# Kernel optimization log

Measured on AMD Instinct MI355X. Metric: run time of the kernel, lower is better.

The kernel has to match this reference:

```python
import jax, jax.numpy as jnp
import numpy as np

N = 100_000      # nodes
E = 1_600_000    # edges (avg degree 16)
D_IN = 128
D_OUT = 128
K = 64           # low-rank attention rank


def setup_inputs() -> dict:
    key = jax.random.key(0)
    ks = jax.random.split(key, 6)
    s = lambda d: 1.0 / np.sqrt(d)
    return {
        "x": jax.random.normal(ks[0], (N, D_IN), dtype=jnp.float32),
        "edge_index": jax.random.randint(ks[1], (2, E), 0, N, dtype=jnp.int32),
        "W_gcn": jax.random.normal(ks[2], (D_IN, D_OUT), dtype=jnp.float32) * s(D_IN),
        "b_gcn": jnp.zeros((D_OUT,), jnp.float32),
        "W_att": jax.random.normal(ks[3], (D_IN, 4 * K), dtype=jnp.float32) * s(D_IN),
        "b_att": jnp.zeros((4 * K,), jnp.float32),
        "W_red": jax.random.normal(ks[4], (D_OUT + 2 * K, D_OUT), dtype=jnp.float32) * s(D_OUT + 2 * K),
        "b_red": jnp.zeros((D_OUT,), jnp.float32),
    }


def _forward(x, W_gcn, b_gcn, W_att, b_att, W_red, b_red, edge_index):
    n = x.shape[0]
    # --- GCN conv (symmetric normalization, self-loops), dropout = identity (eval) ---
    loop = jnp.arange(n, dtype=edge_index.dtype)
    src = jnp.concatenate([edge_index[0], loop])
    dst = jnp.concatenate([edge_index[1], loop])
    deg = jax.ops.segment_sum(jnp.ones_like(dst, dtype=x.dtype), dst, num_segments=n)
    dinv = jax.lax.rsqrt(deg)                      # deg >= 1 due to self-loops
    norm = dinv[src] * dinv[dst]                   # [E+n]
    h = x @ W_gcn                                  # [n, D_OUT]
    agg = jax.ops.segment_sum(h[src] * norm[:, None], dst, num_segments=n) + b_gcn
    x_local = jax.nn.relu(agg)

    # --- Low-rank global attention (LRGA) ---
    t = jax.nn.relu(x @ W_att + b_att)             # [n, 4K]
    U, V, Z, T = jnp.split(t, 4, axis=1)           # each [n, K]
    # joint_normalize2: scalar 1/mean(U @ (V^T @ 1_n))
    D = 1.0 / jnp.mean(U @ (V.T @ jnp.ones((n, 1), x.dtype)))
    res = (U @ (V.T @ Z)) * D                      # [n, K]
    x_global = jnp.concatenate([res, T], axis=1)   # [n, 2K]

    # --- fuse + dim reduce ---
    return jnp.concatenate([x_local, x_global], axis=1) @ W_red + b_red


def reference(x, edge_index, W_gcn, b_gcn, W_att, b_att, W_red, b_red):
    return _forward(x, W_gcn, b_gcn, W_att, b_att, W_red, b_red, edge_index)
```

## Files before the change

### kernel.cpp

```cpp
#include <hip/hip_runtime.h>

#define DIN   128
#define DOUT  128
#define KR    64
#define TCOLS 256
#define WCOLS 384
#define P_RED 1024
#define PSTR  4224
#define STCAP 6144

typedef unsigned short ushort_t;
typedef __attribute__((ext_vector_type(8))) short bf16x8;
typedef __attribute__((ext_vector_type(4))) float f32x4;

__device__ __forceinline__ float bf2f(unsigned short u) {
  return __uint_as_float(((unsigned int)u) << 16);
}
__device__ __forceinline__ unsigned short f2bf(float f) {
  unsigned int b = __float_as_uint(f);
  b = b + 0x7FFFu + ((b >> 16) & 1u);
  return (unsigned short)(b >> 16);
}

__global__ __launch_bounds__(256) void k_init(int* __restrict__ degc, float* __restrict__ VtZ,
                                              float* __restrict__ colsum, int* __restrict__ bcur,
                                              int* __restrict__ ocnt, int N) {
  int i = blockIdx.x * 256 + threadIdx.x;
  if (i < N) degc[i] = 1;
  if (i < 4096) VtZ[i] = 0.f;
  if (i < 128) colsum[i] = 0.f;
  if (i < 128) bcur[i] = 0;
  if (i == 0) ocnt[0] = 0;
}

__global__ __launch_bounds__(256) void k_deg(const int* __restrict__ ei, int* __restrict__ degc, int E) {
  int e = blockIdx.x * 256 + threadIdx.x;
  if (e < E) atomicAdd(&degc[ei[E + e]], 1);
}

__global__ __launch_bounds__(256) void k_split(const float* __restrict__ x,
                                               ushort_t* __restrict__ xhF, ushort_t* __restrict__ xloF,
                                               int N, int total_slots) {
  int gid = blockIdx.x * 256 + threadIdx.x;
  int stride = gridDim.x * 256;
  for (; gid < total_slots; gid += stride) {
    int f = gid >> 6, l = gid & 63;
    int r16 = f >> 2, s = f & 3;
    int row = r16 * 16 + (l & 15);
    int k = s * 32 + ((l >> 4) << 3);
    ushort4 h0, h1, l0, l1;
    if (row < N) {
      float4 a = *(const float4*)&x[(size_t)row * DIN + k];
      float4 b = *(const float4*)&x[(size_t)row * DIN + k + 4];
      h0.x = f2bf(a.x); h0.y = f2bf(a.y); h0.z = f2bf(a.z); h0.w = f2bf(a.w);
      h1.x = f2bf(b.x); h1.y = f2bf(b.y); h1.z = f2bf(b.z); h1.w = f2bf(b.w);
      l0.x = f2bf(a.x - bf2f(h0.x)); l0.y = f2bf(a.y - bf2f(h0.y));
      l0.z = f2bf(a.z - bf2f(h0.z)); l0.w = f2bf(a.w - bf2f(h0.w));
      l1.x = f2bf(b.x - bf2f(h1.x)); l1.y = f2bf(b.y - bf2f(h1.y));
      l1.z = f2bf(b.z - bf2f(h1.z)); l1.w = f2bf(b.w - bf2f(h1.w));
    } else {
      h0 = make_ushort4(0, 0, 0, 0); h1 = h0; l0 = h0; l1 = h0;
    }
    ((ushort4*)xhF)[gid * 2] = h0;
    ((ushort4*)xhF)[gid * 2 + 1] = h1;
    ((ushort4*)xloF)[gid * 2] = l0;
    ((ushort4*)xloF)[gid * 2 + 1] = l1;
  }
}

__global__ __launch_bounds__(256) void k_wprep(const float* __restrict__ Wg, const float* __restrict__ Wa,
                                               ushort_t* __restrict__ whF, ushort_t* __restrict__ wlF) {
  int g = blockIdx.x * 256 + threadIdx.x;
  int f = g >> 6, l = g & 63;
  int c16 = f >> 2, s = f & 3;
  int col = c16 * 16 + (l & 15);
  int k = s * 32 + ((l >> 4) << 3);
#pragma unroll
  for (int j = 0; j < 8; ++j) {
    float v = (col < DOUT) ? Wg[(size_t)(k + j) * DOUT + col]
                           : Wa[(size_t)(k + j) * TCOLS + (col - DOUT)];
    ushort_t h = f2bf(v);
    whF[(size_t)g * 8 + j] = h;
    wlF[(size_t)g * 8 + j] = f2bf(v - bf2f(h));
  }
}

__global__ __launch_bounds__(256) void k_scan1(const int* __restrict__ degc, int* __restrict__ offs,
                                               int* __restrict__ bsums, int N) {
  __shared__ int s[256];
  int tid = threadIdx.x;
  int base = blockIdx.x * 1024 + tid * 4;
  int c[4], e[4];
#pragma unroll
  for (int q = 0; q < 4; ++q) c[q] = (base + q < N) ? (degc[base + q] - 1) : 0;
  e[0] = 0; e[1] = c[0]; e[2] = e[1] + c[1]; e[3] = e[2] + c[2];
  int tsum = e[3] + c[3];
  s[tid] = tsum; __syncthreads();
  for (int off = 1; off < 256; off <<= 1) {
    int v = (tid >= off) ? s[tid - off] : 0;
    __syncthreads();
    s[tid] += v;
    __syncthreads();
  }
  int tb = s[tid] - tsum;
#pragma unroll
  for (int q = 0; q < 4; ++q) if (base + q < N) offs[base + q] = tb + e[q];
  if (tid == 255) bsums[blockIdx.x] = s[255];
}

__global__ __launch_bounds__(128) void k_scan2(const int* __restrict__ bsums, int* __restrict__ boff,
                                               int* __restrict__ offs, int NBLK, int N) {
  __shared__ int s[128];
  int tid = threadIdx.x;
  int v = (tid < NBLK) ? bsums[tid] : 0;
  s[tid] = v; __syncthreads();
  for (int off = 1; off < 128; off <<= 1) {
    int u = (tid >= off) ? s[tid - off] : 0;
    __syncthreads();
    s[tid] += u;
    __syncthreads();
  }
  boff[tid] = s[tid] - v;
  if (tid == 127) offs[N] = s[127];
}

__global__ __launch_bounds__(256) void k_scan3(int* __restrict__ offs, const int* __restrict__ boff,
                                               const int* __restrict__ degc, float* __restrict__ dinv,
                                               int* __restrict__ cursor, int N) {
  int i = blockIdx.x * 256 + threadIdx.x;
  if (i < N) {
    offs[i] += boff[i >> 10];
    dinv[i] = rsqrtf((float)degc[i]);
    cursor[i] = 0;
  }
}

__global__ __launch_bounds__(256) void k_bin(const int* __restrict__ ei, int* __restrict__ bcur,
                                             int2* __restrict__ buckets,
                                             int2* __restrict__ oflow, int* __restrict__ ocnt,
                                             int E, int B, int CAP) {
  __shared__ int hist[128], pref[128], place[128], gbase[128];
  __shared__ int2 st[4096];
  int tid = threadIdx.x;
  int e0 = blockIdx.x * 4096;
  int nE = min(4096, E - e0);
  if (nE <= 0) return;

  if (tid < 128) { hist[tid] = 0; place[tid] = 0; }
  __syncthreads();

  int src[16], dst[16];
#pragma unroll
  for (int q = 0; q < 16; ++q) {
    int idx = tid + q * 256;
    if (idx < nE) {
      src[q] = ei[e0 + idx];
      dst[q] = ei[E + e0 + idx];
      atomicAdd(&hist[dst[q] >> 10], 1);
    }
  }
  __syncthreads();

  if (tid < 128) pref[tid] = hist[tid];
  __syncthreads();
  for (int off = 1; off < 128; off <<= 1) {
    int v = (tid < 128 && tid >= off) ? pref[tid - off] : 0;
    __syncthreads();
    if (tid < 128) pref[tid] += v;
    __syncthreads();
  }
  if (tid < 128) pref[tid] -= hist[tid];
  if (tid < B && hist[tid] > 0) gbase[tid] = atomicAdd(&bcur[tid], hist[tid]);
  __syncthreads();

#pragma unroll
  for (int q = 0; q < 16; ++q) {
    int idx = tid + q * 256;
    if (idx < nE) {
      int b = dst[q] >> 10;
      int p = pref[b] + atomicAdd(&place[b], 1);
      st[p] = make_int2(src[q], dst[q]);
    }
  }
  __syncthreads();

  for (int i = tid; i < nE; i += 256) {
    int2 q = st[i];
    int b = q.y >> 10;
    int gp = gbase[b] + (i - pref[b]);
    if (gp < CAP) {
      buckets[(size_t)b * CAP + gp] = q;
    } else {
      int oi = atomicAdd(ocnt, 1);
      oflow[oi] = q;
    }
  }
}

__global__ __launch_bounds__(256) void k_scatter2(const int2* __restrict__ buckets,
                                                  const int* __restrict__ bcur,
                                                  const int* __restrict__ offs,
                                                  const float* __restrict__ dinv,
                                                  int* __restrict__ cursor,
                                                  int2* __restrict__ csr, int CAP, int N) {
  __shared__ int lcur[256];
  __shared__ int2 st[STCAP];
  int cb = blockIdx.x >> 2;
  int lo = cb * 1024 + (blockIdx.x & 3) * 256;
  if (lo >= N) return;
  int tid = threadIdx.x;
  int nnode = min(256, N - lo);
  int base = offs[lo];
  int nb = offs[lo + nnode] - base;
  if (tid < nnode) lcur[tid] = offs[lo + tid];
  __syncthreads();
  int avail = min(bcur[cb], CAP);
  const int2* sp = &buckets[(size_t)cb * CAP];
  bool staged = (nb <= STCAP);
  int quarter = lo >> 8;
  for (int i = tid; i < avail; i += 256) {
    int2 q = sp[i];
    if ((q.y >> 8) != quarter) continue;
    int p = atomicAdd(&lcur[q.y - lo], 1);
    int2 c;
    c.x = q.x;
    c.y = __float_as_int(dinv[q.x] * dinv[q.y]);
    if (staged) st[p - base] = c;
    else        csr[p] = c;
  }
  __syncthreads();
  if (staged) {
    for (int i = tid; i < nb; i += 256) csr[base + i] = st[i];
  }
  if (tid < nnode) cursor[lo + tid] = lcur[tid];
}

__global__ __launch_bounds__(256) void k_fixup(const int2* __restrict__ oflow, const int* __restrict__ ocnt,
                                               int* __restrict__ cursor, const float* __restrict__ dinv,
                                               int2* __restrict__ csr) {
  int n = ocnt[0];
  for (int i = blockIdx.x * 256 + threadIdx.x; i < n; i += gridDim.x * 256) {
    int2 q = oflow[i];
    int pos = atomicAdd(&cursor[q.y], 1);
    int2 c;
    c.x = q.x;
    c.y = __float_as_int(dinv[q.x] * dinv[q.y]);
    csr[pos] = c;
  }
}

#define LOADK(S, AH, AL, BH, BL)                                              \
  {                                                                           \
    _Pragma("unroll") for (int m_ = 0; m_ < 4; ++m_) {                        \
      size_t fo_ = (((size_t)(r16b + m_) * 4 + (S)) * 64 + lane) * 8;         \
      AH[m_] = *(const bf16x8*)&xhF[fo_];                                     \
      AL[m_] = *(const bf16x8*)&xloF[fo_];                                    \
    }                                                                         \
    _Pragma("unroll") for (int n_ = 0; n_ < 4; ++n_) {                        \
      size_t fo_ = (((size_t)(c16b + n_) * 4 + (S)) * 64 + lane) * 8;         \
      BH[n_] = *(const bf16x8*)&whF[fo_];                                     \
      BL[n_] = *(const bf16x8*)&wlF[fo_];                                     \
    }                                                                         \
  }

__global__ __launch_bounds__(256) void k_gemm1_mfma(const ushort_t* __restrict__ xhF,
                                                    const ushort_t* __restrict__ xloF,
                                                    const ushort_t* __restrict__ whF,
                                                    const ushort_t* __restrict__ wlF,
                                                    const float* __restrict__ ba,
                                                    ushort_t* __restrict__ hs, ushort_t* __restrict__ t,
                                                    int N, int ntiles) {
  int bid = blockIdx.x;
  int g = bid / 24;
  int rem = bid - g * 24;
  int colblk = rem >> 3;
  int ytile = g * 8 + (rem & 7);
  if (ytile >= ntiles) return;

  int tid = threadIdx.x;
  int lane = tid & 63;
  int wave = tid >> 6;
  int wr = wave >> 1, wc = wave & 1;
  int rowbase = ytile * 128 + wr * 64;
  int gcb = colblk * 128 + wc * 64;
  int r16b = ytile * 8 + wr * 4;
  int c16b = colblk * 8 + wc * 4;
  int lr = lane & 15;
  int rq = (lane >> 4) * 4;

  f32x4 acc[4][4] = {};
  bf16x8 ah[2][4], al[2][4], bh[2][4], bl[2][4];

  LOADK(0, ah[0], al[0], bh[0], bl[0]);
#pragma unroll
  for (int s = 0; s < 4; ++s) {
    int cur = s & 1, nxt = cur ^ 1;
    if (s < 3) LOADK(s + 1, ah[nxt], al[nxt], bh[nxt], bl[nxt]);
#pragma unroll
    for (int m = 0; m < 4; ++m)
#pragma unroll
      for (int n = 0; n < 4; ++n) {
        acc[m][n] = __builtin_amdgcn_mfma_f32_16x16x32_bf16(ah[cur][m], bl[cur][n], acc[m][n], 0, 0, 0);
        acc[m][n] = __builtin_amdgcn_mfma_f32_16x16x32_bf16(al[cur][m], bh[cur][n], acc[m][n], 0, 0, 0);
        acc[m][n] = __builtin_amdgcn_mfma_f32_16x16x32_bf16(ah[cur][m], bh[cur][n], acc[m][n], 0, 0, 0);
      }
  }

  if (colblk == 0) {
#pragma unroll
    for (int m = 0; m < 4; ++m)
#pragma unroll
      for (int i = 0; i < 4; ++i) {
        int row = rowbase + m * 16 + rq + i;
        if (row < N) {
#pragma unroll
          for (int n = 0; n < 4; ++n)
            hs[(size_t)row * DOUT + gcb + n * 16 + lr] = f2bf(acc[m][n][i]);
        }
      }
  } else {
    float bav[4];
#pragma unroll
    for (int n = 0; n < 4; ++n) bav[n] = ba[gcb - DOUT + n * 16 + lr];
#pragma unroll
    for (int m = 0; m < 4; ++m)
#pragma unroll
      for (int i = 0; i < 4; ++i) {
        int row = rowbase + m * 16 + rq + i;
        if (row < N) {
#pragma unroll
          for (int n = 0; n < 4; ++n)
            t[(size_t)row * TCOLS + gcb - DOUT + n * 16 + lr] =
                f2bf(fmaxf(acc[m][n][i] + bav[n], 0.f));
        }
      }
  }
}

__global__ __launch_bounds__(256) void k_red(const ushort_t* __restrict__ t, float* __restrict__ part,
                                             int N) {
  __shared__ float csh[512];
  int tid = threadIdx.x;
  int lane = tid & 63;
  int w = tid >> 6;
  int lr = lane & 15;
  int lk = (lane >> 4) * 8;
  int vcol = 64 + w * 16 + lr;
  int col2 = lane * 2;

  f32x4 acc[4] = {};
  float cs0 = 0.f, cs1 = 0.f;
  int ntiles = (N + 31) >> 5;

  for (int tile = blockIdx.x; tile < ntiles; tile += gridDim.x) {
    int r0 = tile * 32;
    const ushort_t* base = &t[(size_t)r0 * TCOLS];
    bf16x8 a, b[4];
    if (r0 + 32 <= N) {
#pragma unroll
      for (int j = 0; j < 8; ++j)
        ((short*)&a)[j] = (short)base[(size_t)(lk + j) * TCOLS + vcol];
#pragma unroll
      for (int n = 0; n < 4; ++n)
#pragma unroll
        for (int j = 0; j < 8; ++j)
          ((short*)&b[n])[j] = (short)base[(size_t)(lk + j) * TCOLS + 128 + n * 16 + lr];
#pragma unroll
      for (int j = 0; j < 8; ++j) {
        ushort2 u = *(const ushort2*)&base[(size_t)(w * 8 + j) * TCOLS + col2];
        cs0 += bf2f(u.x); cs1 += bf2f(u.y);
      }
    } else {
#pragma unroll
      for (int j = 0; j < 8; ++j) {
        int r = r0 + lk + j;
        ((short*)&a)[j] = (r < N) ? (short)t[(size_t)r * TCOLS + vcol] : (short)0;
      }
#pragma unroll
      for (int n = 0; n < 4; ++n)
#pragma unroll
        for (int j = 0; j < 8; ++j) {
          int r = r0 + lk + j;
          ((short*)&b[n])[j] = (r < N) ? (short)t[(size_t)r * TCOLS + 128 + n * 16 + lr] : (short)0;
        }
#pragma unroll
      for (int j = 0; j < 8; ++j) {
        int r = r0 + w * 8 + j;
        if (r < N) {
          ushort2 u = *(const ushort2*)&t[(size_t)r * TCOLS + col2];
          cs0 += bf2f(u.x); cs1 += bf2f(u.y);
        }
      }
    }
#pragma unroll
    for (int n = 0; n < 4; ++n)
      acc[n] = __builtin_amdgcn_mfma_f32_16x16x32_bf16(a, b[n], acc[n], 0, 0, 0);
  }

  float* pb = &part[(size_t)blockIdx.x * PSTR];
  int rq = (lane >> 4) * 4;
#pragma unroll
  for (int n = 0; n < 4; ++n)
#pragma unroll
    for (int i = 0; i < 4; ++i)
      pb[(w * 16 + rq + i) * 64 + n * 16 + lr] = acc[n][i];

  csh[tid] = cs0;
  csh[256 + tid] = cs1;
  __syncthreads();
  if (w == 0) {
    float t0 = csh[lane] + csh[64 + lane] + csh[128 + lane] + csh[192 + lane];
    float t1 = csh[256 + lane] + csh[320 + lane] + csh[384 + lane] + csh[448 + lane];
    pb[4096 + col2] = t0;
    pb[4096 + col2 + 1] = t1;
  }
}

__global__ __launch_bounds__(256) void k_redsum(const float* __restrict__ part,
                                                float* __restrict__ VtZ, float* __restrict__ colsum) {
  __shared__ float s[256];
  int tid = threadIdx.x;
  int j = blockIdx.x * 64 + (tid & 63);
  int bc = tid >> 6;
  float a = 0.f;
#pragma unroll 4
  for (int b = bc; b < P_RED; b += 4) a += part[(size_t)b * PSTR + j];
  s[tid] = a;
  __syncthreads();
  if (bc == 0) {
    float v = s[tid] + s[tid + 64] + s[tid + 128] + s[tid + 192];
    if (j < 4096) VtZ[j] = v;
    else colsum[j - 4096] = v;
  }
}

__global__ __launch_bounds__(64) void k_d(const float* __restrict__ colsum, float* __restrict__ Dws, int N) {
  __shared__ float s[64];
  int k = threadIdx.x;
  s[k] = colsum[k] * colsum[64 + k];
  __syncthreads();
  for (int off = 32; off > 0; off >>= 1) {
    if (k < off) s[k] += s[k + off];
    __syncthreads();
  }
  if (k == 0) {
    float p = s[0];
    Dws[0] = (p != 0.f) ? ((float)N / p) : 0.f;
  }
}

__global__ __launch_bounds__(256) void k_prep(const float* __restrict__ VtZ,
                                              const float* __restrict__ Dws,
                                              const float* __restrict__ Wr,
                                              ushort_t* __restrict__ weffT) {
  int c = blockIdx.x;
  int k = threadIdx.x;
  float v;
  if (k < 128 || k >= 192) {
    v = Wr[(size_t)k * DOUT + c];
  } else {
    float Dv = Dws[0];
    int kk = k - 128;
    float acc = 0.f;
#pragma unroll 8
    for (int j = 0; j < 64; ++j)
      acc += VtZ[kk * 64 + j] * Wr[(size_t)(128 + j) * DOUT + c];
    v = acc * Dv;
  }
  weffT[(size_t)c * 256 + k] = f2bf(v);
}

__global__ __launch_bounds__(256) void k_out_mfma(const ushort_t* __restrict__ xl,
                                                  const ushort_t* __restrict__ t,
                                                  const ushort_t* __restrict__ weffT,
                                                  const float* __restrict__ br,
                                                  float* __restrict__ out, int N) {
  int tid = threadIdx.x;
  int lane = tid & 63;
  int wave = tid >> 6;
  int wr = wave >> 1, wc = wave & 1;
  int rowbase = blockIdx.x * 128 + wr * 64;
  int cbase = wc * 64;
  int lr = lane & 15;
  int lk = (lane >> 4) * 8;

  int rows[4];
#pragma unroll
  for (int m = 0; m < 4; ++m) {
    int r = rowbase + m * 16 + lr;
    rows[m] = (r < N) ? r : (N - 1);
  }

  f32x4 acc[4][4] = {};

#pragma unroll
  for (int s = 0; s < 8; ++s) {
    int k0 = s * 32 + lk;
    bf16x8 a[4], b[4];
#pragma unroll
    for (int m = 0; m < 4; ++m) {
      const ushort_t* ap;
      if (s < 4)      ap = &xl[(size_t)rows[m] * DOUT + k0];
      else if (s < 6) ap = &t[(size_t)rows[m] * TCOLS + (k0 - 128)];
      else            ap = &t[(size_t)rows[m] * TCOLS + k0];
      a[m] = *(const bf16x8*)ap;
    }
#pragma unroll
    for (int n = 0; n < 4; ++n) {
      int c = cbase + n * 16 + lr;
      b[n] = *(const bf16x8*)&weffT[(size_t)c * 256 + k0];
    }
#pragma unroll
    for (int m = 0; m < 4; ++m)
#pragma unroll
      for (int n = 0; n < 4; ++n)
        acc[m][n] = __builtin_amdgcn_mfma_f32_16x16x32_bf16(a[m], b[n], acc[m][n], 0, 0, 0);
  }

  float brv[4];
#pragma unroll
  for (int n = 0; n < 4; ++n) brv[n] = br[cbase + n * 16 + lr];

  int rq = (lane >> 4) * 4;
#pragma unroll
  for (int m = 0; m < 4; ++m) {
#pragma unroll
    for (int i = 0; i < 4; ++i) {
      int row = rowbase + m * 16 + rq + i;
      if (row < N) {
#pragma unroll
        for (int n = 0; n < 4; ++n)
          out[(size_t)row * DOUT + cbase + n * 16 + lr] = acc[m][n][i] + brv[n];
      }
    }
  }
}

__global__ __launch_bounds__(256) void k_aggn(const ushort_t* __restrict__ hs, const int2* __restrict__ csr,
                                              const int* __restrict__ offs, const float* __restrict__ dinv,
                                              const float* __restrict__ bg,
                                              ushort_t* __restrict__ xl, int N) {
  int node = blockIdx.x * 4 + (threadIdx.x >> 6);
  int lane = threadIdx.x & 63;
  if (node >= N) return;
  int c2 = 2 * lane;
  float dn = dinv[node];
  ushort2 u = *(const ushort2*)&hs[(size_t)node * DOUT + c2];
  float a0 = dn * dn * bf2f(u.x);
  float a1 = dn * dn * bf2f(u.y);
  int e = offs[node], e1 = offs[node + 1];
  for (; e + 4 <= e1; e += 4) {
    int2 q0 = csr[e], q1 = csr[e + 1], q2 = csr[e + 2], q3 = csr[e + 3];
    ushort2 r0 = *(const ushort2*)&hs[(size_t)q0.x * DOUT + c2];
    ushort2 r1 = *(const ushort2*)&hs[(size_t)q1.x * DOUT + c2];
    ushort2 r2 = *(const ushort2*)&hs[(size_t)q2.x * DOUT + c2];
    ushort2 r3 = *(const ushort2*)&hs[(size_t)q3.x * DOUT + c2];
    float n0 = __int_as_float(q0.y), n1 = __int_as_float(q1.y);
    float n2 = __int_as_float(q2.y), n3 = __int_as_float(q3.y);
    a0 += n0 * bf2f(r0.x) + n1 * bf2f(r1.x) + n2 * bf2f(r2.x) + n3 * bf2f(r3.x);
    a1 += n0 * bf2f(r0.y) + n1 * bf2f(r1.y) + n2 * bf2f(r2.y) + n3 * bf2f(r3.y);
  }
  for (; e < e1; ++e) {
    int2 q = csr[e];
    ushort2 r = *(const ushort2*)&hs[(size_t)q.x * DOUT + c2];
    float n0 = __int_as_float(q.y);
    a0 += n0 * bf2f(r.x);
    a1 += n0 * bf2f(r.y);
  }
  ushort2 o;
  o.x = f2bf(fmaxf(a0 + bg[c2], 0.f));
  o.y = f2bf(fmaxf(a1 + bg[c2 + 1], 0.f));
  *(ushort2*)&xl[(size_t)node * DOUT + c2] = o;
}

extern "C" void kernel_launch(void* const* d_in, const int* in_sizes, int n_in,
                              void* d_out, int out_size, void* d_ws, size_t ws_size,
                              hipStream_t stream) {
  const float* x  = (const float*)d_in[0];
  const int* ei   = (const int*)d_in[1];
  const float* Wg = (const float*)d_in[2];
  const float* bg = (const float*)d_in[3];
  const float* Wa = (const float*)d_in[4];
  const float* ba = (const float*)d_in[5];
  const float* Wr = (const float*)d_in[6];
  const float* br = (const float*)d_in[7];
  float* out = (float*)d_out;

  const int N = in_sizes[0] / DIN;
  const int E = in_sizes[1] / 2;

  const int NT128 = (N + 127) / 128;
  const int N16P = NT128 * 8;
  const int NFRAG_A = N16P * 4;
  const int B = (N + 1023) >> 10;
  const int CAP = ((E / (B > 0 ? B : 1)) * 3 / 2 + 255) & ~255;

  char* p = (char*)d_ws;
  auto alloc = [&](size_t bytes) {
    char* r = p;
    p += (bytes + 255) & ~(size_t)255;
    return r;
  };
  float* Dws    = (float*)alloc(256);
  float* colsum = (float*)alloc(128 * 4);
  float* VtZ    = (float*)alloc(4096 * 4);
  int*   bsums  = (int*)alloc(1024);
  int*   boff   = (int*)alloc(1024);
  int*   bcur   = (int*)alloc(1024);
  int*   ocnt   = (int*)alloc(256);
  ushort_t* weffT = (ushort_t*)alloc(128 * 256 * 2);
  ushort_t* whF = (ushort_t*)alloc((size_t)24 * 4 * 512 * 2);
  ushort_t* wlF = (ushort_t*)alloc((size_t)24 * 4 * 512 * 2);
  float* part   = (float*)alloc((size_t)P_RED * PSTR * 4);
  int*   degc   = (int*)alloc((size_t)N * 4);
  float* dinv   = (float*)alloc((size_t)N * 4);
  int*   offs   = (int*)alloc((size_t)(N + 1) * 4);
  int*   cursor = (int*)alloc((size_t)N * 4);
  int2*  csr    = (int2*)alloc((size_t)E * 8);
  int2*  buckets= (int2*)alloc((size_t)B * CAP * 8);
  int2*  oflow  = (int2*)alloc((size_t)E * 8);
  ushort_t* xhF = (ushort_t*)alloc((size_t)NFRAG_A * 512 * 2);
  ushort_t* xloF= (ushort_t*)alloc((size_t)NFRAG_A * 512 * 2);
  ushort_t* hs  = (ushort_t*)alloc((size_t)N * DOUT * 2);
  ushort_t* t   = (ushort_t*)alloc((size_t)N * TCOLS * 2);
  ushort_t* xl  = (ushort_t*)alloc((size_t)N * DOUT * 2);
  (void)ws_size; (void)n_in; (void)out_size;

  const int GN = (N + 255) / 256;
  const int GE = (E + 255) / 256;
  const int NBLK = (N + 1023) / 1024;
  const int G1 = ((NT128 + 7) / 8) * 24;
  const int GBIN = (E + 4095) / 4096;

  k_init<<<GN, 256, 0, stream>>>(degc, VtZ, colsum, bcur, ocnt, N);
  k_deg<<<GE, 256, 0, stream>>>(ei, degc, E);
  k_split<<<2048, 256, 0, stream>>>(x, xhF, xloF, N, NFRAG_A * 64);
  k_wprep<<<24, 256, 0, stream>>>(Wg, Wa, whF, wlF);
  k_scan1<<<NBLK, 256, 0, stream>>>(degc, offs, bsums, N);
  k_scan2<<<1, 128, 0, stream>>>(bsums, boff, offs, NBLK, N);
  k_scan3<<<GN, 256, 0, stream>>>(offs, boff, degc, dinv, cursor, N);
  k_bin<<<GBIN, 256, 0, stream>>>(ei, bcur, buckets, oflow, ocnt, E, B, CAP);
  k_scatter2<<<B * 4, 256, 0, stream>>>(buckets, bcur, offs, dinv, cursor, csr, CAP, N);
  k_fixup<<<32, 256, 0, stream>>>(oflow, ocnt, cursor, dinv, csr);
  k_gemm1_mfma<<<G1, 256, 0, stream>>>(xhF, xloF, whF, wlF, ba, hs, t, N, NT128);
  k_red<<<P_RED, 256, 0, stream>>>(t, part, N);
  k_redsum<<<PSTR / 64, 256, 0, stream>>>(part, VtZ, colsum);
  k_d<<<1, 64, 0, stream>>>(colsum, Dws, N);
  k_prep<<<128, 256, 0, stream>>>(VtZ, Dws, Wr, weffT);
  k_aggn<<<(N + 3) / 4, 256, 0, stream>>>(hs, csr, offs, dinv, bg, xl, N);
  k_out_mfma<<<(N + 127) / 128, 256, 0, stream>>>(xl, t, weffT, br, out, N);
}
```

Baseline: 450.8 us.

## Stage row tiles in LDS for reduction and output GEMM, prepack weights as fragments

Measured after the change: 446.0 us. Within noise of the previous version (-1.1%).

```diff
diff --git a/kernel.cpp b/kernel.cpp
--- a/kernel.cpp
+++ b/kernel.cpp
@@ -339,6 +339,7 @@
 
 __global__ __launch_bounds__(256) void k_red(const ushort_t* __restrict__ t, float* __restrict__ part,
                                              int N) {
+  __shared__ ushort_t ts[32 * 200];
   __shared__ float csh[512];
   int tid = threadIdx.x;
   int lane = tid & 63;
@@ -354,47 +355,38 @@
 
   for (int tile = blockIdx.x; tile < ntiles; tile += gridDim.x) {
     int r0 = tile * 32;
-    const ushort_t* base = &t[(size_t)r0 * TCOLS];
+    for (int i = tid; i < 768; i += 256) {
+      int r = i / 24, c0 = (i % 24) * 8;
+      int row = r0 + r;
+      ushort4 v0, v1;
+      if (row < N) {
+        v0 = ((const ushort4*)&t[(size_t)row * TCOLS + c0])[0];
+        v1 = ((const ushort4*)&t[(size_t)row * TCOLS + c0])[1];
+      } else {
+        v0 = make_ushort4(0, 0, 0, 0); v1 = v0;
+      }
+      *(ushort4*)&ts[r * 200 + c0] = v0;
+      *(ushort4*)&ts[r * 200 + c0 + 4] = v1;
+    }
+    __syncthreads();
     bf16x8 a, b[4];
-    if (r0 + 32 <= N) {
+#pragma unroll
+    for (int j = 0; j < 8; ++j)
+      ((ushort_t*)&a)[j] = ts[(lk + j) * 200 + vcol];
+#pragma unroll
+    for (int n = 0; n < 4; ++n)
 #pragma unroll
       for (int j = 0; j < 8; ++j)
-        ((short*)&a)[j] = (short)base[(size_t)(lk + j) * TCOLS + vcol];
-#pragma unroll
-      for (int n = 0; n < 4; ++n)
-#pragma unroll
-        for (int j = 0; j < 8; ++j)
-          ((short*)&b[n])[j] = (short)base[(size_t)(lk + j) * TCOLS + 128 + n * 16 + lr];
-#pragma unroll
-      for (int j = 0; j < 8; ++j) {
-        ushort2 u = *(const ushort2*)&base[(size_t)(w * 8 + j) * TCOLS + col2];
-        cs0 += bf2f(u.x); cs1 += bf2f(u.y);
-      }
-    } else {
-#pragma unroll
-      for (int j = 0; j < 8; ++j) {
-        int r = r0 + lk + j;
-        ((short*)&a)[j] = (r < N) ? (short)t[(size_t)r * TCOLS + vcol] : (short)0;
-      }
-#pragma unroll
-      for (int n = 0; n < 4; ++n)
-#pragma unroll
-        for (int j = 0; j < 8; ++j) {
-          int r = r0 + lk + j;
-          ((short*)&b[n])[j] = (r < N) ? (short)t[(size_t)r * TCOLS + 128 + n * 16 + lr] : (short)0;
-        }
-#pragma unroll
-      for (int j = 0; j < 8; ++j) {
-        int r = r0 + w * 8 + j;
-        if (r < N) {
-          ushort2 u = *(const ushort2*)&t[(size_t)r * TCOLS + col2];
-          cs0 += bf2f(u.x); cs1 += bf2f(u.y);
-        }
-      }
+        ((ushort_t*)&b[n])[j] = ts[(lk + j) * 200 + 128 + n * 16 + lr];
+#pragma unroll
+    for (int j = 0; j < 8; ++j) {
+      ushort2 u = *(const ushort2*)&ts[(w * 8 + j) * 200 + col2];
+      cs0 += bf2f(u.x); cs1 += bf2f(u.y);
     }
 #pragma unroll
     for (int n = 0; n < 4; ++n)
       acc[n] = __builtin_amdgcn_mfma_f32_16x16x32_bf16(a, b[n], acc[n], 0, 0, 0);
+    __syncthreads();
   }
 
   float* pb = &part[(size_t)blockIdx.x * PSTR];
@@ -452,88 +444,96 @@
 __global__ __launch_bounds__(256) void k_prep(const float* __restrict__ VtZ,
                                               const float* __restrict__ Dws,
                                               const float* __restrict__ Wr,
-                                              ushort_t* __restrict__ weffT) {
-  int c = blockIdx.x;
-  int k = threadIdx.x;
-  float v;
-  if (k < 128 || k >= 192) {
-    v = Wr[(size_t)k * DOUT + c];
-  } else {
-    float Dv = Dws[0];
-    int kk = k - 128;
-    float acc = 0.f;
-#pragma unroll 8
-    for (int j = 0; j < 64; ++j)
-      acc += VtZ[kk * 64 + j] * Wr[(size_t)(128 + j) * DOUT + c];
-    v = acc * Dv;
-  }
-  weffT[(size_t)c * 256 + k] = f2bf(v);
+                                              ushort_t* __restrict__ weffF) {
+  int g = blockIdx.x * 256 + threadIdx.x;
+  int f = g >> 6, l = g & 63;
+  int c16 = f >> 3, s = f & 7;
+  int c = c16 * 16 + (l & 15);
+  int k0 = s * 32 + ((l >> 4) << 3);
+  float Dv = Dws[0];
+#pragma unroll
+  for (int j = 0; j < 8; ++j) {
+    int k = k0 + j;
+    float v;
+    if (k < 128 || k >= 192) {
+      v = Wr[(size_t)k * DOUT + c];
+    } else {
+      int kk = k - 128;
+      float acc = 0.f;
+      for (int q = 0; q < 64; ++q)
+        acc += VtZ[kk * 64 + q] * Wr[(size_t)(128 + q) * DOUT + c];
+      v = acc * Dv;
+    }
+    weffF[(size_t)g * 8 + j] = f2bf(v);
+  }
 }
 
 __global__ __launch_bounds__(256) void k_out_mfma(const ushort_t* __restrict__ xl,
                                                   const ushort_t* __restrict__ t,
-                                                  const ushort_t* __restrict__ weffT,
+                                                  const ushort_t* __restrict__ weffF,
                                                   const float* __restrict__ br,
                                                   float* __restrict__ out, int N) {
+  __shared__ ushort_t ys[32 * 264];
   int tid = threadIdx.x;
   int lane = tid & 63;
-  int wave = tid >> 6;
-  int wr = wave >> 1, wc = wave & 1;
-  int rowbase = blockIdx.x * 128 + wr * 64;
-  int cbase = wc * 64;
+  int w = tid >> 6;
   int lr = lane & 15;
   int lk = (lane >> 4) * 8;
-
-  int rows[4];
-#pragma unroll
-  for (int m = 0; m < 4; ++m) {
-    int r = rowbase + m * 16 + lr;
-    rows[m] = (r < N) ? r : (N - 1);
-  }
-
-  f32x4 acc[4][4] = {};
-
+  int rq = (lane >> 4) * 4;
+  int r0 = blockIdx.x * 32;
+
+  for (int i = tid; i < 1024; i += 256) {
+    int r = i >> 5, c0 = (i & 31) * 8;
+    int row = r0 + r;
+    ushort4 v0, v1;
+    if (row < N) {
+      const ushort_t* src;
+      if (c0 < 128)      src = &xl[(size_t)row * DOUT + c0];
+      else if (c0 < 192) src = &t[(size_t)row * TCOLS + (c0 - 128)];
+      else               src = &t[(size_t)row * TCOLS + c0];
+      v0 = ((const ushort4*)src)[0];
+      v1 = ((const ushort4*)src)[1];
+    } else {
+      v0 = make_ushort4(0, 0, 0, 0); v1 = v0;
+    }
+    *(ushort4*)&ys[r * 264 + c0] = v0;
+    *(ushort4*)&ys[r * 264 + c0 + 4] = v1;
+  }
+  __syncthreads();
+
+  f32x4 acc[2][2] = {};
 #pragma unroll
   for (int s = 0; s < 8; ++s) {
-    int k0 = s * 32 + lk;
-    bf16x8 a[4], b[4];
-#pragma unroll
-    for (int m = 0; m < 4; ++m) {
-      const ushort_t* ap;
-      if (s < 4)      ap = &xl[(size_t)rows[m] * DOUT + k0];
-      else if (s < 6) ap = &t[(size_t)rows[m] * TCOLS + (k0 - 128)];
-      else            ap = &t[(size_t)rows[m] * TCOLS + k0];
-      a[m] = *(const bf16x8*)ap;
-    }
-#pragma unroll
-    for (int n = 0; n < 4; ++n) {
-      int c = cbase + n * 16 + lr;
-      b[n] = *(const bf16x8*)&weffT[(size_t)c * 256 + k0];
-    }
-#pragma unroll
-    for (int m = 0; m < 4; ++m)
-#pragma unroll
-      for (int n = 0; n < 4; ++n)
+    bf16x8 a[2], b[2];
+#pragma unroll
+    for (int m = 0; m < 2; ++m)
+      a[m] = *(const bf16x8*)&ys[(m * 16 + lr) * 264 + s * 32 + lk];
+#pragma unroll
+    for (int n = 0; n < 2; ++n) {
+      int f = (w * 2 + n) * 8 + s;
+      b[n] = *(const bf16x8*)&weffF[((size_t)f * 64 + lane) * 8];
+    }
+#pragma unroll
+    for (int m = 0; m < 2; ++m)
+#pragma unroll
+      for (int n = 0; n < 2; ++n)
         acc[m][n] = __builtin_amdgcn_mfma_f32_16x16x32_bf16(a[m], b[n], acc[m][n], 0, 0, 0);
   }
 
-  float brv[4];
-#pragma unroll
-  for (int n = 0; n < 4; ++n) brv[n] = br[cbase + n * 16 + lr];
-
-  int rq = (lane >> 4) * 4;
-#pragma unroll
-  for (int m = 0; m < 4; ++m) {
+  float brv[2];
+#pragma unroll
+  for (int n = 0; n < 2; ++n) brv[n] = br[w * 32 + n * 16 + lr];
+#pragma unroll
+  for (int m = 0; m < 2; ++m)
 #pragma unroll
     for (int i = 0; i < 4; ++i) {
-      int row = rowbase + m * 16 + rq + i;
+      int row = r0 + m * 16 + rq + i;
       if (row < N) {
 #pragma unroll
-        for (int n = 0; n < 4; ++n)
-          out[(size_t)row * DOUT + cbase + n * 16 + lr] = acc[m][n][i] + brv[n];
+        for (int n = 0; n < 2; ++n)
+          out[(size_t)row * DOUT + w * 32 + n * 16 + lr] = acc[m][n][i] + brv[n];
       }
     }
-  }
 }
 
 __global__ __launch_bounds__(256) void k_aggn(const ushort_t* __restrict__ hs, const int2* __restrict__ csr,
@@ -608,7 +608,7 @@
   int*   boff   = (int*)alloc(1024);
   int*   bcur   = (int*)alloc(1024);
   int*   ocnt   = (int*)alloc(256);
-  ushort_t* weffT = (ushort_t*)alloc(128 * 256 * 2);
+  ushort_t* weffF = (ushort_t*)alloc(128 * 256 * 2);
   ushort_t* whF = (ushort_t*)alloc((size_t)24 * 4 * 512 * 2);
   ushort_t* wlF = (ushort_t*)alloc((size_t)24 * 4 * 512 * 2);
   float* part   = (float*)alloc((size_t)P_RED * PSTR * 4);
@@ -631,6 +631,7 @@
   const int NBLK = (N + 1023) / 1024;
   const int G1 = ((NT128 + 7) / 8) * 24;
   const int GBIN = (E + 4095) / 4096;
+  const int NT32 = (N + 31) / 32;
 
   k_init<<<GN, 256, 0, stream>>>(degc, VtZ, colsum, bcur, ocnt, N);
   k_deg<<<GE, 256, 0, stream>>>(ei, degc, E);
@@ -646,7 +647,7 @@
   k_red<<<P_RED, 256, 0, stream>>>(t, part, N);
   k_redsum<<<PSTR / 64, 256, 0, stream>>>(part, VtZ, colsum);
   k_d<<<1, 64, 0, stream>>>(colsum, Dws, N);
-  k_prep<<<128, 256, 0, stream>>>(VtZ, Dws, Wr, weffT);
+  k_prep<<<16, 256, 0, stream>>>(VtZ, Dws, Wr, weffF);
   k_aggn<<<(N + 3) / 4, 256, 0, stream>>>(hs, csr, offs, dinv, bg, xl, N);
-  k_out_mfma<<<(N + 127) / 128, 256, 0, stream>>>(xl, t, weffT, br, out, N);
-}
+  k_out_mfma<<<NT32, 256, 0, stream>>>(xl, t, weffF, br, out, N);
+}
```
